# Optimization experiments

Measured on AMD Instinct MI355X. Metric: run time of the kernel, lower is better.

The kernel has to match this reference:

```python
import jax, jax.numpy as jnp
import numpy as np

ROUTING_ITERS = 3
EPS = 1e-8


def squash(x):
    # scale = ||x||^2 / (1 + ||x||^2); out = scale * x / (||x|| + eps)
    norm = jnp.linalg.norm(x, axis=-1, keepdims=True)
    scale = norm ** 2 / (1.0 + norm ** 2)
    return scale * x / (norm + EPS)


def setup_inputs() -> dict:
    key = jax.random.key(0)
    kx, kw = jax.random.split(key)
    B, R, C, IC, OC = 256, 1152, 10, 8, 16
    x = jax.random.normal(kx, (B, R, IC), dtype=jnp.float32)
    # learned prediction weights: [1, num_routes, num_capsules, in_ch, out_ch]
    weights = jax.random.normal(kw, (1, R, C, IC, OC), dtype=jnp.float32)
    return {"x": x, "weights": weights}


def reference(x, weights):
    # prediction vectors u_hat[b,r,c,o] = sum_i x[b,r,i] * W[r,c,i,o]
    u = jnp.einsum('bri,rcio->brco', x, weights[0])  # [B,R,C,OC]
    b = jnp.zeros(u.shape[:3], dtype=u.dtype)        # routing logits [B,R,C]
    v = jnp.zeros(u.shape[:1] + u.shape[2:], dtype=u.dtype)
    for _ in range(ROUTING_ITERS):
        c = jax.nn.softmax(b, axis=-1)               # coupling coeffs over capsules
        s = jnp.einsum('brc,brco->bco', c, u)        # weighted sum over routes
        v = squash(s)                                # [B,C,OC]
        b = b + jnp.einsum('brco,bco->brc', u, v)    # agreement update
    return v
```

## Files before the change

kernel.cpp:

```cpp
#include <hip/hip_runtime.h>
#include <cstdint>
#include <cstddef>

#define NB 256
#define NR 1152
#define NC 10
#define NI 8
#define NO 16
#define NSPLIT 2
#define NSWEEP 9
#define NRC 144

static __device__ __forceinline__ uint32_t bf16_pack2(float lo, float hi) {
    uint32_t vl = __float_as_uint(lo);
    vl = vl + 0x7FFFu + ((vl >> 16) & 1u);
    uint32_t vh = __float_as_uint(hi);
    vh = vh + 0x7FFFu + ((vh >> 16) & 1u);
    return (vl >> 16) | (vh & 0xFFFF0000u);
}

__global__ __launch_bounds__(320) void caps_u_s1_kernel(
    const float* __restrict__ x, const float* __restrict__ W,
    uint32_t* __restrict__ u, uint32_t* __restrict__ part1)
{
    const int t  = threadIdx.x;
    const int c  = t >> 5;
    const int rl = (t & 31) >> 2;
    const int oq = t & 3;
    const int rc = blockIdx.x >> 4;
    const int bg = blockIdx.x & 15;
    const int b0 = bg * 16;
    const int r  = rc * 8 + rl;

    __shared__ float xs[16][8][8];

    if (t < 256) {
        const int bi = t >> 4, rem = t & 15;
        const int rr = rem >> 1, hf = rem & 1;
        *(float4*)&xs[bi][rr][hf * 4] =
            *(const float4*)(x + ((size_t)(b0 + bi) * NR + rc * 8 + rr) * 8 + hf * 4);
    }

    const float* wb = W + ((size_t)r * NC + c) * (NI * NO) + oq * 4;
    float4 wf[8];
#pragma unroll
    for (int i = 0; i < 8; ++i) wf[i] = *(const float4*)(wb + i * NO);

    __syncthreads();

#pragma unroll 2
    for (int bi = 0; bi < 16; ++bi) {
        const float4 xv4a = *(const float4*)&xs[bi][rl][0];
        const float4 xv4b = *(const float4*)&xs[bi][rl][4];
        const float xr[8] = {xv4a.x, xv4a.y, xv4a.z, xv4a.w,
                             xv4b.x, xv4b.y, xv4b.z, xv4b.w};
        float ax = 0.f, ay = 0.f, az = 0.f, aw = 0.f;
#pragma unroll
        for (int i = 0; i < 8; ++i) {
            const float xv = xr[i];
            ax = fmaf(xv, wf[i].x, ax); ay = fmaf(xv, wf[i].y, ay);
            az = fmaf(xv, wf[i].z, az); aw = fmaf(xv, wf[i].w, aw);
        }
        uint2 s;
        s.x = bf16_pack2(ax, ay);
        s.y = bf16_pack2(az, aw);
        *(uint2*)(u + (((size_t)(b0 + bi) * NC + c) * NR + r) * 8 + oq * 2) = s;

        float sx = ax, sy = ay, sz = az, sw = aw;
#pragma unroll
        for (int off = 4; off <= 16; off <<= 1) {
            sx += __shfl_xor(sx, off); sy += __shfl_xor(sy, off);
            sz += __shfl_xor(sz, off); sw += __shfl_xor(sw, off);
        }
        if ((t & 28) == 0) {
            uint2 p;
            p.x = bf16_pack2(sx, sy);
            p.y = bf16_pack2(sz, sw);
            *(uint2*)(part1 + ((size_t)(b0 + bi) * NRC + rc) * 80
                      + c * 8 + oq * 2) = p;
        }
    }
}

__global__ __launch_bounds__(256, 2) void caps_pass_kernel(
    const uint32_t* __restrict__ u, const uint32_t* __restrict__ part1,
    float* __restrict__ vsum, const float* __restrict__ part_prev,
    float* __restrict__ partout)
{
    const int b  = blockIdx.x >> 1;
    const int sp = blockIdx.x & 1;
    const int t  = threadIdx.x;
    const int oq = t & 3;
    const int rl = t >> 2;

    __shared__ float vss[160];
    __shared__ float sred[4][160];

    if (t < 160) {
        float v;
        if (part_prev != nullptr) {
            const float s = part_prev[(size_t)b * 160 + t]
                          + part_prev[((size_t)NB + b) * 160 + t];
            float n2 = s * s;
            n2 += __shfl_xor(n2, 1);
            n2 += __shfl_xor(n2, 2);
            n2 += __shfl_xor(n2, 4);
            n2 += __shfl_xor(n2, 8);
            const float nrm = sqrtf(n2);
            v = vsum[(size_t)b * 160 + t]
              + s * (n2 / (1.f + n2) / (nrm + 1e-8f));
        } else {
            const uint32_t* p = part1 + (size_t)b * NRC * 80 + (t >> 1);
            const bool hi = t & 1;
            float s0 = 0.f, s1 = 0.f, s2 = 0.f, s3 = 0.f;
#pragma unroll 4
            for (int g = 0; g < NRC; g += 4) {
                const uint32_t w0 = p[(g + 0) * 80];
                const uint32_t w1 = p[(g + 1) * 80];
                const uint32_t w2 = p[(g + 2) * 80];
                const uint32_t w3 = p[(g + 3) * 80];
                s0 += hi ? __uint_as_float(w0 & 0xFFFF0000u) : __uint_as_float(w0 << 16);
                s1 += hi ? __uint_as_float(w1 & 0xFFFF0000u) : __uint_as_float(w1 << 16);
                s2 += hi ? __uint_as_float(w2 & 0xFFFF0000u) : __uint_as_float(w2 << 16);
                s3 += hi ? __uint_as_float(w3 & 0xFFFF0000u) : __uint_as_float(w3 << 16);
            }
            const float s = 0.1f * ((s0 + s1) + (s2 + s3));
            float n2 = s * s;
            n2 += __shfl_xor(n2, 1);
            n2 += __shfl_xor(n2, 2);
            n2 += __shfl_xor(n2, 4);
            n2 += __shfl_xor(n2, 8);
            const float nrm = sqrtf(n2);
            v = s * (n2 / (1.f + n2) / (nrm + 1e-8f));
            vsum[(size_t)b * 160 + t] = v;
        }
        vss[t] = v;
    }
    __syncthreads();

    float acc[10][4];
#pragma unroll
    for (int c = 0; c < 10; ++c)
#pragma unroll
        for (int j = 0; j < 4; ++j) acc[c][j] = 0.f;

    const uint2* ub = (const uint2*)u + (size_t)b * NC * NR * 4 + oq;

    for (int k = 0; k < NSWEEP; ++k) {
        const int r = sp * (NSWEEP * 64) + k * 64 + rl;
        uint2 q[10];
#pragma unroll
        for (int c = 0; c < 10; ++c) q[c] = ub[((size_t)c * NR + r) * 4];

        float lg[10];
#pragma unroll
        for (int c = 0; c < 10; ++c) {
            const float4 vq = *(const float4*)&vss[c * 16 + oq * 4];
            float d = __uint_as_float(q[c].x << 16) * vq.x;
            d = fmaf(__uint_as_float(q[c].x & 0xFFFF0000u), vq.y, d);
            d = fmaf(__uint_as_float(q[c].y << 16),         vq.z, d);
            d = fmaf(__uint_as_float(q[c].y & 0xFFFF0000u), vq.w, d);
            lg[c] = d;
        }
#pragma unroll
        for (int c = 0; c < 10; ++c) {
            lg[c] += __shfl_xor(lg[c], 1);
            lg[c] += __shfl_xor(lg[c], 2);
        }
        float m = lg[0];
#pragma unroll
        for (int c = 1; c < 10; ++c) m = fmaxf(m, lg[c]);
        float wgt[10], ssum = 0.f;
#pragma unroll
        for (int c = 0; c < 10; ++c) { wgt[c] = __expf(lg[c] - m); ssum += wgt[c]; }
        const float inv = 1.f / ssum;
#pragma unroll
        for (int c = 0; c < 10; ++c) {
            const float wv = wgt[c] * inv;
            acc[c][0] = fmaf(wv, __uint_as_float(q[c].x << 16),         acc[c][0]);
            acc[c][1] = fmaf(wv, __uint_as_float(q[c].x & 0xFFFF0000u), acc[c][1]);
            acc[c][2] = fmaf(wv, __uint_as_float(q[c].y << 16),         acc[c][2]);
            acc[c][3] = fmaf(wv, __uint_as_float(q[c].y & 0xFFFF0000u), acc[c][3]);
        }
    }

#pragma unroll
    for (int off = 4; off <= 32; off <<= 1)
#pragma unroll
        for (int c = 0; c < 10; ++c)
#pragma unroll
            for (int j = 0; j < 4; ++j) acc[c][j] += __shfl_xor(acc[c][j], off);

    const int wv = t >> 6;
    if ((t & 63) < 4) {
#pragma unroll
        for (int c = 0; c < 10; ++c)
#pragma unroll
            for (int j = 0; j < 4; ++j)
                sred[wv][c * 16 + oq * 4 + j] = acc[c][j];
    }
    __syncthreads();

    if (t < 160) {
        partout[((size_t)sp * NB + b) * 160 + t]
            = sred[0][t] + sred[1][t] + sred[2][t] + sred[3][t];
    }
}

__global__ __launch_bounds__(192) void caps_final_kernel(
    const float* __restrict__ p2b, float* __restrict__ out)
{
    const int b = blockIdx.x;
    const int t = threadIdx.x;
    if (t >= 160) return;
    const float s = p2b[(size_t)b * 160 + t]
                  + p2b[((size_t)NB + b) * 160 + t];
    float n2 = s * s;
    n2 += __shfl_xor(n2, 1);
    n2 += __shfl_xor(n2, 2);
    n2 += __shfl_xor(n2, 4);
    n2 += __shfl_xor(n2, 8);
    const float nrm   = sqrtf(n2);
    const float scale = n2 / (1.f + n2) / (nrm + 1e-8f);
    out[(size_t)b * 160 + t] = scale * s;
}

extern "C" void kernel_launch(void* const* d_in, const int* in_sizes, int n_in,
                              void* d_out, int out_size, void* d_ws, size_t ws_size,
                              hipStream_t stream) {
    const float* x = (const float*)d_in[0];
    const float* W = (const float*)d_in[1];
    float* out = (float*)d_out;

    uint8_t*  ws   = (uint8_t*)d_ws;
    uint32_t* u    = (uint32_t*)ws;
    uint32_t* prt1 = (uint32_t*)(ws + 94371840u);
    float*    p2a  = (float*)(ws + 94371840u + 11796480u);
    float*    p2b  = (float*)(ws + 94371840u + 11796480u + 327680u);
    float*    vsm  = (float*)(ws + 94371840u + 11796480u + 655360u);

    caps_u_s1_kernel<<<2304, 320, 0, stream>>>(x, W, u, prt1);
    caps_pass_kernel<<<NB * NSPLIT, 256, 0, stream>>>(u, prt1, vsm, nullptr, p2a);
    caps_pass_kernel<<<NB * NSPLIT, 256, 0, stream>>>(u, nullptr, vsm, p2a, p2b);
    caps_final_kernel<<<NB, 192, 0, stream>>>(p2b, out);
}
```

Before: 138.2 us.

## Split routing pass three ways and load 8 bf16 per thread with uint4

The routing pass kernel now splits routes across three blocks per batch instead of two. Each thread handles 8 output channels through 16-byte loads in place of 4 channels through 8-byte loads, so two lanes instead of four cover a route and 128 routes are processed per sweep. The aim is more blocks in flight and wider memory transactions when streaming the large bf16 u tensor. In exchange, the accumulator arrays double in size, which raises register pressure, and the partial-sum buffers and the final reductions grow to three slices.

```diff
diff --git a/kernel.cpp b/kernel.cpp
--- a/kernel.cpp
+++ b/kernel.cpp
@@ -7,8 +7,8 @@
 #define NC 10
 #define NI 8
 #define NO 16
-#define NSPLIT 2
-#define NSWEEP 9
+#define NSPLIT 3
+#define NSWEEP 3
 #define NRC 144
 
 static __device__ __forceinline__ uint32_t bf16_pack2(float lo, float hi) {
@@ -87,11 +87,11 @@
     float* __restrict__ vsum, const float* __restrict__ part_prev,
     float* __restrict__ partout)
 {
-    const int b  = blockIdx.x >> 1;
-    const int sp = blockIdx.x & 1;
+    const int b  = blockIdx.x / NSPLIT;
+    const int sp = blockIdx.x % NSPLIT;
     const int t  = threadIdx.x;
-    const int oq = t & 3;
-    const int rl = t >> 2;
+    const int oh = t & 1;
+    const int rl = t >> 1;
 
     __shared__ float vss[160];
     __shared__ float sred[4][160];
@@ -100,7 +100,8 @@
         float v;
         if (part_prev != nullptr) {
             const float s = part_prev[(size_t)b * 160 + t]
-                          + part_prev[((size_t)NB + b) * 160 + t];
+                          + part_prev[((size_t)NB + b) * 160 + t]
+                          + part_prev[((size_t)2 * NB + b) * 160 + t];
             float n2 = s * s;
             n2 += __shfl_xor(n2, 1);
             n2 += __shfl_xor(n2, 2);
@@ -138,35 +139,38 @@
     }
     __syncthreads();
 
-    float acc[10][4];
+    float acc[10][8];
 #pragma unroll
     for (int c = 0; c < 10; ++c)
 #pragma unroll
-        for (int j = 0; j < 4; ++j) acc[c][j] = 0.f;
-
-    const uint2* ub = (const uint2*)u + (size_t)b * NC * NR * 4 + oq;
+        for (int j = 0; j < 8; ++j) acc[c][j] = 0.f;
+
+    const uint4* ub = (const uint4*)u + ((size_t)b * NC * NR) * 2 + oh;
 
     for (int k = 0; k < NSWEEP; ++k) {
-        const int r = sp * (NSWEEP * 64) + k * 64 + rl;
-        uint2 q[10];
-#pragma unroll
-        for (int c = 0; c < 10; ++c) q[c] = ub[((size_t)c * NR + r) * 4];
+        const int r = sp * (NSWEEP * 128) + k * 128 + rl;
+        uint4 q[10];
+#pragma unroll
+        for (int c = 0; c < 10; ++c) q[c] = ub[((size_t)c * NR + r) * 2];
 
         float lg[10];
 #pragma unroll
         for (int c = 0; c < 10; ++c) {
-            const float4 vq = *(const float4*)&vss[c * 16 + oq * 4];
-            float d = __uint_as_float(q[c].x << 16) * vq.x;
-            d = fmaf(__uint_as_float(q[c].x & 0xFFFF0000u), vq.y, d);
-            d = fmaf(__uint_as_float(q[c].y << 16),         vq.z, d);
-            d = fmaf(__uint_as_float(q[c].y & 0xFFFF0000u), vq.w, d);
+            const float4 va = *(const float4*)&vss[c * 16 + oh * 8];
+            const float4 vb = *(const float4*)&vss[c * 16 + oh * 8 + 4];
+            float d = __uint_as_float(q[c].x << 16) * va.x;
+            d = fmaf(__uint_as_float(q[c].x & 0xFFFF0000u), va.y, d);
+            d = fmaf(__uint_as_float(q[c].y << 16),         va.z, d);
+            d = fmaf(__uint_as_float(q[c].y & 0xFFFF0000u), va.w, d);
+            d = fmaf(__uint_as_float(q[c].z << 16),         vb.x, d);
+            d = fmaf(__uint_as_float(q[c].z & 0xFFFF0000u), vb.y, d);
+            d = fmaf(__uint_as_float(q[c].w << 16),         vb.z, d);
+            d = fmaf(__uint_as_float(q[c].w & 0xFFFF0000u), vb.w, d);
             lg[c] = d;
         }
 #pragma unroll
-        for (int c = 0; c < 10; ++c) {
+        for (int c = 0; c < 10; ++c)
             lg[c] += __shfl_xor(lg[c], 1);
-            lg[c] += __shfl_xor(lg[c], 2);
-        }
         float m = lg[0];
 #pragma unroll
         for (int c = 1; c < 10; ++c) m = fmaxf(m, lg[c]);
@@ -181,23 +185,29 @@
             acc[c][1] = fmaf(wv, __uint_as_float(q[c].x & 0xFFFF0000u), acc[c][1]);
             acc[c][2] = fmaf(wv, __uint_as_float(q[c].y << 16),         acc[c][2]);
             acc[c][3] = fmaf(wv, __uint_as_float(q[c].y & 0xFFFF0000u), acc[c][3]);
-        }
-    }
-
-#pragma unroll
-    for (int off = 4; off <= 32; off <<= 1)
+            acc[c][4] = fmaf(wv, __uint_as_float(q[c].z << 16),         acc[c][4]);
+            acc[c][5] = fmaf(wv, __uint_as_float(q[c].z & 0xFFFF0000u), acc[c][5]);
+            acc[c][6] = fmaf(wv, __uint_as_float(q[c].w << 16),         acc[c][6]);
+            acc[c][7] = fmaf(wv, __uint_as_float(q[c].w & 0xFFFF0000u), acc[c][7]);
+        }
+    }
+
+#pragma unroll
+    for (int off = 2; off <= 32; off <<= 1)
 #pragma unroll
         for (int c = 0; c < 10; ++c)
 #pragma unroll
-            for (int j = 0; j < 4; ++j) acc[c][j] += __shfl_xor(acc[c][j], off);
+            for (int j = 0; j < 8; ++j) acc[c][j] += __shfl_xor(acc[c][j], off);
 
     const int wv = t >> 6;
-    if ((t & 63) < 4) {
-#pragma unroll
-        for (int c = 0; c < 10; ++c)
-#pragma unroll
-            for (int j = 0; j < 4; ++j)
-                sred[wv][c * 16 + oq * 4 + j] = acc[c][j];
+    if ((t & 62) == 0) {
+#pragma unroll
+        for (int c = 0; c < 10; ++c) {
+            *(float4*)&sred[wv][c * 16 + oh * 8] =
+                make_float4(acc[c][0], acc[c][1], acc[c][2], acc[c][3]);
+            *(float4*)&sred[wv][c * 16 + oh * 8 + 4] =
+                make_float4(acc[c][4], acc[c][5], acc[c][6], acc[c][7]);
+        }
     }
     __syncthreads();
 
@@ -214,7 +224,8 @@
     const int t = threadIdx.x;
     if (t >= 160) return;
     const float s = p2b[(size_t)b * 160 + t]
-                  + p2b[((size_t)NB + b) * 160 + t];
+                  + p2b[((size_t)NB + b) * 160 + t]
+                  + p2b[((size_t)2 * NB + b) * 160 + t];
     float n2 = s * s;
     n2 += __shfl_xor(n2, 1);
     n2 += __shfl_xor(n2, 2);
@@ -236,8 +247,8 @@
     uint32_t* u    = (uint32_t*)ws;
     uint32_t* prt1 = (uint32_t*)(ws + 94371840u);
     float*    p2a  = (float*)(ws + 94371840u + 11796480u);
-    float*    p2b  = (float*)(ws + 94371840u + 11796480u + 327680u);
-    float*    vsm  = (float*)(ws + 94371840u + 11796480u + 655360u);
+    float*    p2b  = (float*)(ws + 94371840u + 11796480u + 491520u);
+    float*    vsm  = (float*)(ws + 94371840u + 11796480u + 983040u);
 
     caps_u_s1_kernel<<<2304, 320, 0, stream>>>(x, W, u, prt1);
     caps_pass_kernel<<<NB * NSPLIT, 256, 0, stream>>>(u, prt1, vsm, nullptr, p2a);
```

New measurement: 161.1 us. 16.6% more time.
